# Kernel optimization log

Measured on AMD Instinct MI355X. Metric: run time of the kernel, lower is better.

## Reference

```python
import jax, jax.numpy as jnp
import numpy as np

MARGIN = 0.2


def _pairwise_distances(emb):
    # Euclidean distances with torch-style zero-masked sqrt (non-squared path).
    dot = jnp.matmul(emb, emb.T)                      # [N, N]
    sq = jnp.diagonal(dot)                            # [N]
    d2 = sq[None, :] - 2.0 * dot + sq[:, None]
    d2 = jnp.maximum(d2, 0.0)
    zero_mask = (d2 == 0.0).astype(d2.dtype)
    return (1.0 - zero_mask) * jnp.sqrt(d2 + zero_mask * 1e-16)


def setup_inputs() -> dict:
    key = jax.random.key(0)
    k1, k2 = jax.random.split(key)
    N, D, C = 512, 512, 64
    labels = jax.random.randint(k1, (N,), 0, C, dtype=jnp.int64 if jax.config.jax_enable_x64 else jnp.int32)
    embeddings = jax.random.normal(k2, (N, D), dtype=jnp.float32)
    return {"labels": labels, "embeddings": embeddings}


def reference(labels, embeddings):
    # Semi-hard... actually Difficulty.Easy path of TripletLoss.forward
    N = embeddings.shape[0]
    pdist = _pairwise_distances(embeddings)                      # [N, N]
    adjacency_not = labels[None, :] != labels[:, None]           # [N, N] bool

    pdist_tile = jnp.tile(pdist, (N, 1))                         # [N*N, N]
    mask = jnp.tile(adjacency_not, (N, 1))                       # [N*N, N]
    # Easy difficulty: negatives strictly farther than the anchor-positive dist
    mask = mask & (pdist_tile > pdist.T.reshape(-1, 1))

    maskf = mask.astype(pdist.dtype)
    mask_final = (jnp.sum(maskf, axis=1, keepdims=True) > 0.0).reshape(N, N).T  # [N, N] bool

    # masked minimum over tiled rows
    axis_max = jnp.max(pdist_tile, axis=1, keepdims=True)
    neg_outside = (jnp.min((pdist_tile - axis_max) * maskf, axis=1, keepdims=True)
                   + axis_max).reshape(N, N).T                   # [N, N]

    # masked maximum over negatives per anchor
    adjf = adjacency_not.astype(pdist.dtype)
    axis_min = jnp.min(pdist, axis=1, keepdims=True)
    neg_inside = jnp.max((pdist - axis_min) * adjf, axis=1, keepdims=True) + axis_min  # [N, 1]
    neg_inside = jnp.broadcast_to(neg_inside, (N, N))

    semi_hard_negatives = jnp.where(mask_final, neg_outside, neg_inside)
    loss_mat = MARGIN + pdist - semi_hard_negatives

    eye = jnp.eye(N, dtype=bool)
    mask_positives = (labels[None, :] == labels[:, None]) & ~eye
    num_positives = jnp.sum(mask_positives).astype(loss_mat.dtype)
    loss = jnp.sum(jnp.maximum(loss_mat * mask_positives.astype(loss_mat.dtype), 0.0))
    return loss / (num_positives + 1e-8)
```

## Files before the change

kernel.cpp:

```cpp
#include <hip/hip_runtime.h>
#include <math.h>


#define NN 512
#define MARGIN_F 0.2f
#define LK 528

typedef __attribute__((ext_vector_type(8))) short bf16x8;
typedef __attribute__((ext_vector_type(4))) float f32x4;

__device__ __forceinline__ unsigned short f2bf(float x){
    unsigned u = __float_as_uint(x);
    return (unsigned short)((u + 0x7FFFu + ((u >> 16) & 1u)) >> 16);
}
__device__ __forceinline__ float bf2f(unsigned short h){
    return __uint_as_float(((unsigned)h) << 16);
}

#define SH_OFF   0
#define SNI_OFF  135168
#define SNJ_OFF  135296
#define SCR_OFF  135424
#define SM_BYTES 139520

__global__ __launch_bounds__(512) void k_dist(
    const float* __restrict__ emb,
    float* __restrict__ Dm,
    int* __restrict__ ctrl)
{
    __shared__ __align__(16) char sm[SM_BYTES];
    short* sh  = (short*)(sm + SH_OFF);
    float* snI = (float*)(sm + SNI_OFF);
    float* snJ = (float*)(sm + SNJ_OFF);
    f32x4* scr = (f32x4*)(sm + SCR_OFF);

    const int tid  = threadIdx.x;
    const int wave = tid >> 6, lane = tid & 63;
    const int bi = blockIdx.y, bj = blockIdx.x;

    if (bi == 0 && bj == 0 && tid < 3) ctrl[tid] = 0;

    {
        const int row = tid >> 3;
        const int s8  = tid & 7;
        const int isJ = row >> 5;
        const int rl  = row & 31;
        const int grow = (isJ ? bj : bi) * 32 + rl;
        const int bhi = (isJ << 1), blo = bhi + 1;
        const float4* Ep = (const float4*)emb;
        float ss = 0.f;
        #pragma unroll
        for (int i = 0; i < 16; ++i) {
            const int c4 = s8 + (i << 3);
            const float4 v = Ep[(size_t)grow * 128 + c4];
            ss = fmaf(v.x, v.x, ss); ss = fmaf(v.y, v.y, ss);
            ss = fmaf(v.z, v.z, ss); ss = fmaf(v.w, v.w, ss);
            ushort4 h, l;
            h.x = f2bf(v.x); l.x = f2bf(v.x - bf2f(h.x));
            h.y = f2bf(v.y); l.y = f2bf(v.y - bf2f(h.y));
            h.z = f2bf(v.z); l.z = f2bf(v.z - bf2f(h.z));
            h.w = f2bf(v.w); l.w = f2bf(v.w - bf2f(h.w));
            *(ushort4*)(&sh[(bhi * 32 + rl) * LK + (c4 << 2)]) = h;
            *(ushort4*)(&sh[(blo * 32 + rl) * LK + (c4 << 2)]) = l;
        }
        ss += __shfl_xor(ss, 1, 64);
        ss += __shfl_xor(ss, 2, 64);
        ss += __shfl_xor(ss, 4, 64);
        if (s8 == 0) { if (isJ) snJ[rl] = ss; else snI[rl] = ss; }
    }
    __syncthreads();

    const int quad = wave & 3, khalf = wave >> 2;
    const int rowb = (quad >> 1) << 4, colb = (quad & 1) << 4;
    const int fr = lane & 15;
    const int k0 = (lane >> 4) << 3;
    f32x4 acc = {0.f, 0.f, 0.f, 0.f};
    #pragma unroll
    for (int t8 = 0; t8 < 8; ++t8) {
        const int k = k0 + (((khalf << 3) + t8) << 5);
        const bf16x8 ahi = *(const bf16x8*)(&sh[(0 * 32 + rowb + fr) * LK + k]);
        const bf16x8 alo = *(const bf16x8*)(&sh[(1 * 32 + rowb + fr) * LK + k]);
        const bf16x8 bhi = *(const bf16x8*)(&sh[(2 * 32 + colb + fr) * LK + k]);
        const bf16x8 blo = *(const bf16x8*)(&sh[(3 * 32 + colb + fr) * LK + k]);
        acc = __builtin_amdgcn_mfma_f32_16x16x32_bf16(ahi, bhi, acc, 0, 0, 0);
        acc = __builtin_amdgcn_mfma_f32_16x16x32_bf16(ahi, blo, acc, 0, 0, 0);
        acc = __builtin_amdgcn_mfma_f32_16x16x32_bf16(alo, bhi, acc, 0, 0, 0);
    }
    if (khalf == 1) scr[quad * 64 + lane] = acc;
    __syncthreads();
    if (khalf == 0) {
        const f32x4 other = scr[quad * 64 + lane];
        acc[0] += other[0]; acc[1] += other[1];
        acc[2] += other[2]; acc[3] += other[3];
        const int colg = bj * 32 + colb + fr;
        const float sc = snJ[colb + fr];
        const int rl0 = rowb + ((lane >> 4) << 2);
        #pragma unroll
        for (int reg = 0; reg < 4; ++reg) {
            const int rl = rl0 + reg;
            const float d2 = snI[rl] + sc - 2.f * acc[reg];
            Dm[(size_t)(bi * 32 + rl) * NN + colg] = sqrtf(fmaxf(d2, 0.f));
        }
    }
}

__global__ __launch_bounds__(256) void k_mine(
    const int* __restrict__ labels,
    const float* __restrict__ Dm,
    float* __restrict__ accums,
    float* __restrict__ out,
    int nblocks)
{
    __shared__ int slbl[NN];
    __shared__ float drow[4][NN];
    __shared__ unsigned short plist[4][128];
    __shared__ int pcnt[4];

    const int tid = threadIdx.x, wave = tid >> 6, lane = tid & 63;
    const int j = blockIdx.x * 4 + wave;

    slbl[tid] = labels[tid];
    slbl[tid + 256] = labels[tid + 256];
    if (tid < 4) pcnt[tid] = 0;
    __syncthreads();

    const float4* rp = (const float4*)(Dm + (size_t)j * NN);
    const float4 va = rp[lane * 2], vb = rp[lane * 2 + 1];
    *(float4*)(&drow[wave][lane * 8]) = va;
    *(float4*)(&drow[wave][lane * 8 + 4]) = vb;
    float d[8] = {va.x, va.y, va.z, va.w, vb.x, vb.y, vb.z, vb.w};
    const int lj = slbl[j];
    int lb[8];
    #pragma unroll
    for (int m = 0; m < 8; ++m) lb[m] = slbl[lane * 8 + m];

    #pragma unroll
    for (int m = 0; m < 8; ++m){
        const int k = lane * 8 + m;
        if (k != j && lb[m] == lj){
            const int ix = atomicAdd(&pcnt[wave], 1);
            plist[wave][ix] = (unsigned short)k;
        }
    }
    float vmaxl = 0.f;
    #pragma unroll
    for (int m = 0; m < 8; ++m) if (lb[m] != lj) vmaxl = fmaxf(vmaxl, d[m]);
    #pragma unroll
    for (int o = 32; o > 0; o >>= 1) vmaxl = fmaxf(vmaxl, __shfl_xor(vmaxl, o, 64));

    const int np = pcnt[wave];
    float wloss = 0.f;
    for (int p = 0; p < np; ++p){
        const int a = plist[wave][p];
        const float dpa = drow[wave][a];
        float vm = 1e30f;
        #pragma unroll
        for (int m = 0; m < 8; ++m){
            const bool cnd = (lb[m] != lj) && (d[m] > dpa);
            vm = cnd ? fminf(vm, d[m]) : vm;
        }
        #pragma unroll
        for (int o = 32; o > 0; o >>= 1) vm = fminf(vm, __shfl_xor(vm, o, 64));
        const float neg = (vm < 1e29f) ? vm : vmaxl;
        const float term = MARGIN_F + dpa - neg;
        if (lane == 0 && term > 0.f) wloss += term;
    }
    if (lane == 0){
        if (wloss != 0.f) atomicAdd(&accums[0], wloss);
        if (np) atomicAdd((unsigned int*)&accums[1], (unsigned int)np);
    }
    __syncthreads();
    if (tid == 0){
        __threadfence();
        const unsigned old = atomicAdd((unsigned int*)&accums[2], 1u);
        if (old == (unsigned)(nblocks - 1)){
            const float L = atomicAdd(&accums[0], 0.f);
            const unsigned C = atomicAdd((unsigned int*)&accums[1], 0u);
            out[0] = L / ((float)C + 1e-8f);
        }
    }
}

extern "C" void kernel_launch(void* const* d_in, const int* in_sizes, int n_in,
                              void* d_out, int out_size, void* d_ws, size_t ws_size,
                              hipStream_t stream) {
    (void)in_sizes; (void)n_in; (void)out_size; (void)ws_size;
    const int* labels = (const int*)d_in[0];
    const float* emb  = (const float*)d_in[1];
    char* ws = (char*)d_ws;
    float* Dm   = (float*)ws;
    int*   ctrl = (int*)(ws + (1u << 20));

    k_dist<<<dim3(16, 16), 512, 0, stream>>>(emb, Dm, ctrl);
    k_mine<<<128, 256, 0, stream>>>(labels, Dm, (float*)ctrl, (float*)d_out, 128);
}
```

Measured before the change: 77.57 us.

## Exploit distance matrix symmetry by computing only upper-triangular tiles

The distance kernel now launches only the 136 upper-triangular 32x32 tiles instead of all 256. Each block writes its tile and also its mirrored tile, transposed through a small shared-memory buffer. This roughly halves the MFMA and embedding-load work, at the cost of extra LDS, a transpose step, and a small per-block loop to map the block index to a tile. Diagonal blocks write the same values twice, and the mirrored result is only exactly symmetric if the hi/lo split MFMA products are symmetric, so tiny asymmetries could change the mining comparisons.

```diff
diff --git a/kernel.cpp b/kernel.cpp
--- a/kernel.cpp
+++ b/kernel.cpp
@@ -21,7 +21,8 @@
 #define SNI_OFF  135168
 #define SNJ_OFF  135296
 #define SCR_OFF  135424
-#define SM_BYTES 139520
+#define TRP_OFF  139520
+#define SM_BYTES 143872
 
 __global__ __launch_bounds__(512) void k_dist(
     const float* __restrict__ emb,
@@ -33,12 +34,21 @@
     float* snI = (float*)(sm + SNI_OFF);
     float* snJ = (float*)(sm + SNJ_OFF);
     f32x4* scr = (f32x4*)(sm + SCR_OFF);
+    float* trp = (float*)(sm + TRP_OFF);
 
     const int tid  = threadIdx.x;
     const int wave = tid >> 6, lane = tid & 63;
-    const int bi = blockIdx.y, bj = blockIdx.x;
-
-    if (bi == 0 && bj == 0 && tid < 3) ctrl[tid] = 0;
+
+    int t = blockIdx.x, bi = 0;
+    #pragma unroll
+    for (int r = 0; r < 16; ++r) {
+        const int rowlen = 16 - r;
+        if (t < rowlen) { bi = r; break; }
+        t -= rowlen;
+    }
+    const int bj = bi + t;
+
+    if (blockIdx.x == 0 && tid < 3) ctrl[tid] = 0;
 
     {
         const int row = tid >> 3;
@@ -73,7 +83,8 @@
     const int quad = wave & 3, khalf = wave >> 2;
     const int rowb = (quad >> 1) << 4, colb = (quad & 1) << 4;
     const int fr = lane & 15;
-    const int k0 = (lane >> 4) << 3;
+    const int q4 = lane >> 4;
+    const int k0 = q4 << 3;
     f32x4 acc = {0.f, 0.f, 0.f, 0.f};
     #pragma unroll
     for (int t8 = 0; t8 < 8; ++t8) {
@@ -94,12 +105,25 @@
         acc[2] += other[2]; acc[3] += other[3];
         const int colg = bj * 32 + colb + fr;
         const float sc = snJ[colb + fr];
-        const int rl0 = rowb + ((lane >> 4) << 2);
+        const int rl0 = rowb + (q4 << 2);
+        float dv[4];
         #pragma unroll
         for (int reg = 0; reg < 4; ++reg) {
             const int rl = rl0 + reg;
             const float d2 = snI[rl] + sc - 2.f * acc[reg];
-            Dm[(size_t)(bi * 32 + rl) * NN + colg] = sqrtf(fmaxf(d2, 0.f));
+            dv[reg] = sqrtf(fmaxf(d2, 0.f));
+            Dm[(size_t)(bi * 32 + rl) * NN + colg] = dv[reg];
+        }
+        float* T = trp + quad * (16 * 17);
+        #pragma unroll
+        for (int reg = 0; reg < 4; ++reg)
+            T[fr * 17 + (q4 << 2) + reg] = dv[reg];
+        #pragma unroll
+        for (int reg = 0; reg < 4; ++reg) {
+            const float m = T[((q4 << 2) + reg) * 17 + fr];
+            const int mrow = bj * 32 + colb + (q4 << 2) + reg;
+            const int mcol = bi * 32 + rowb + fr;
+            Dm[(size_t)mrow * NN + mcol] = m;
         }
     }
 }
@@ -191,6 +215,6 @@
     float* Dm   = (float*)ws;
     int*   ctrl = (int*)(ws + (1u << 20));
 
-    k_dist<<<dim3(16, 16), 512, 0, stream>>>(emb, Dm, ctrl);
+    k_dist<<<136, 512, 0, stream>>>(emb, Dm, ctrl);
     k_mine<<<128, 256, 0, stream>>>(labels, Dm, (float*)ctrl, (float*)d_out, 128);
 }
```

New measurement: 76.70 us. About the same (-1.1%).
